# Performance work log

Hardware: AMD Instinct MI355X
Metric: run time of the kernel (lower is better)

Reference implementation:

```python
import jax, jax.numpy as jnp
import numpy as np

B, T, I = 8, 8192, 512
E, K, J = 16, 1024, 512

def setup_inputs() -> dict:
    key = jax.random.key(0)
    k1, k2, k3 = jax.random.split(key, 3)
    x = jax.random.normal(k1, (B, T, I), dtype=jnp.float32)
    Ind = jax.random.randint(k2, (B, E, K), 0, T, dtype=jnp.int32)
    bound = 1.0 / np.sqrt(I)
    W = jax.random.uniform(k3, (E, I, J), dtype=jnp.float32, minval=-bound, maxval=bound)
    return {"x": x, "Ind": Ind, "W": W}

def reference(x, Ind, W):
    # gather: [B,E,K,I] = x[b, Ind[b,e,k], :]
    gathered = jnp.take_along_axis(x[:, None, :, :], Ind[:, :, :, None], axis=2)
    # per-expert GEMM: [B,E,K,J]
    return jnp.einsum('beki,eij->bekj', gathered, W)
```

## Files before the change

### kernel.cpp

```cpp
#include <hip/hip_runtime.h>
#include <stdint.h>

typedef short short8 __attribute__((ext_vector_type(8)));
typedef float floatx16 __attribute__((ext_vector_type(16)));

constexpr int CB = 8;
constexpr int CT = 8192;
constexpr int CI = 512;
constexpr int CE = 16;
constexpr int CK = 1024;
constexpr int CJ = 512;

__device__ __forceinline__ uint32_t f2bf(float f) {
    union { float f; uint32_t u; } c; c.f = f;
    return (c.u + 0x7fffu + ((c.u >> 16) & 1u)) >> 16;
}
__device__ __forceinline__ uint32_t pack2(float lo, float hi) {
    return f2bf(lo) | (f2bf(hi) << 16);
}

__global__ __launch_bounds__(256, 2) void eg_kernel(
    const float* __restrict__ x, const int* __restrict__ Ind,
    const float* __restrict__ W, float* __restrict__ out)
{
    constexpr int AS_STRIDE = 20;
    constexpr int BS_STRIDE = 132;

    __shared__ __align__(16) uint32_t As[128 * AS_STRIDE];
    __shared__ __align__(16) uint32_t Bs[16 * BS_STRIDE];
    __shared__ int s_idx[128];

    const int t = threadIdx.x;
    const int z = blockIdx.z;
    const int e = z & (CE - 1);
    const int b = z >> 4;
    const int mtile = blockIdx.y;
    const int ntile = blockIdx.x;

    if (t < 128) s_idx[t] = Ind[z * CK + mtile * 128 + t];
    __syncthreads();

    const int am = t >> 1;
    const int ah = t & 1;
    const float* aptr = x + ((size_t)b * CT + s_idx[am]) * CI + ah * 16;
    uint32_t* adst = &As[am * AS_STRIDE + ah * 8];

    const int bjc = t & 31;
    const int bkp = t >> 5;
    const float* wptr = W + (size_t)e * CI * CJ + ntile * 128 + bjc * 4;

    const int ln = t & 63, wv = t >> 6;
    const int wm = (wv >> 1) * 64, wn = (wv & 1) * 64;
    const int lrow = ln & 31;
    const int lh = ln >> 5;

    const floatx16 fz = {0.f,0.f,0.f,0.f,0.f,0.f,0.f,0.f,0.f,0.f,0.f,0.f,0.f,0.f,0.f,0.f};
    floatx16 acc[2][2] = {{fz, fz}, {fz, fz}};

    for (int kt = 0; kt < CI / 32; ++kt) {
        {
            const float4* ap = (const float4*)(aptr + kt * 32);
            float4 a0 = ap[0], a1 = ap[1], a2 = ap[2], a3 = ap[3];
            uint4 w0 = make_uint4(pack2(a0.x, a0.y), pack2(a0.z, a0.w),
                                  pack2(a1.x, a1.y), pack2(a1.z, a1.w));
            uint4 w1 = make_uint4(pack2(a2.x, a2.y), pack2(a2.z, a2.w),
                                  pack2(a3.x, a3.y), pack2(a3.z, a3.w));
            ((uint4*)adst)[0] = w0;
            *((uint4*)(adst + 4)) = w1;
        }
        #pragma unroll
        for (int i = 0; i < 2; ++i) {
            const int kp = bkp + i * 8;
            const float* wp = wptr + (size_t)(kt * 32 + kp * 2) * CJ;
            float4 r0 = *(const float4*)(wp);
            float4 r1 = *(const float4*)(wp + CJ);
            uint4 wq = make_uint4(pack2(r0.x, r1.x), pack2(r0.y, r1.y),
                                  pack2(r0.z, r1.z), pack2(r0.w, r1.w));
            *((uint4*)&Bs[kp * BS_STRIDE + bjc * 4]) = wq;
        }
        __syncthreads();

        #pragma unroll
        for (int sub = 0; sub < 2; ++sub) {
            short8 af[2], bf[2];
            #pragma unroll
            for (int mt = 0; mt < 2; ++mt)
                af[mt] = *(const short8*)&As[(wm + mt * 32 + lrow) * AS_STRIDE + sub * 8 + lh * 4];
            #pragma unroll
            for (int nt = 0; nt < 2; ++nt) {
                const int n = wn + nt * 32 + lrow;
                const int kp0 = sub * 8 + lh * 4;
                union { uint32_t u[4]; short8 s; } cv;
                cv.u[0] = Bs[(kp0 + 0) * BS_STRIDE + n];
                cv.u[1] = Bs[(kp0 + 1) * BS_STRIDE + n];
                cv.u[2] = Bs[(kp0 + 2) * BS_STRIDE + n];
                cv.u[3] = Bs[(kp0 + 3) * BS_STRIDE + n];
                bf[nt] = cv.s;
            }
            #pragma unroll
            for (int mt = 0; mt < 2; ++mt)
                #pragma unroll
                for (int nt = 0; nt < 2; ++nt)
                    acc[mt][nt] = __builtin_amdgcn_mfma_f32_32x32x16_bf16(
                        af[mt], bf[nt], acc[mt][nt], 0, 0, 0);
        }
        __syncthreads();
    }

    const size_t obase = (size_t)z * CK * CJ;
    #pragma unroll
    for (int mt = 0; mt < 2; ++mt) {
        const int gm0 = mtile * 128 + wm + mt * 32 + lh * 4;
        #pragma unroll
        for (int nt = 0; nt < 2; ++nt) {
            const int gn = ntile * 128 + wn + nt * 32 + lrow;
            #pragma unroll
            for (int r = 0; r < 16; ++r) {
                const int gm = gm0 + (r & 3) + 8 * (r >> 2);
                out[obase + (size_t)gm * CJ + gn] = acc[mt][nt][r];
            }
        }
    }
}

extern "C" void kernel_launch(void* const* d_in, const int* in_sizes, int n_in,
                              void* d_out, int out_size, void* d_ws, size_t ws_size,
                              hipStream_t stream) {
    const float* x   = (const float*)d_in[0];
    const int*   Ind = (const int*)d_in[1];
    const float* W   = (const float*)d_in[2];
    float* out = (float*)d_out;

    dim3 grid(CJ / 128, CK / 128, CB * CE);
    dim3 block(256);
    hipLaunchKernelGGL(eg_kernel, grid, block, 0, stream, x, Ind, W, out);
}
```

Measured before the change: 510.8 us.

## Pre-convert inputs to bf16 and stream tiles via direct global-to-LDS loads

Adds two pre-pass kernels that convert x and W to bf16 in every call, with W repacked into a K-pair-interleaved tile layout. The GEMM kernel then loads 64-wide K tiles straight into LDS with global_load_lds, using an XOR swizzle on the A tile to avoid bank conflicts, and does fewer synchronisations per K step. This removes the per-tile fp32 loads and conversions in the main kernel and halves the bytes it reads. In exchange, a full pass converting x (128 MB) and W runs on every call, and the launch bound is raised to 4 blocks per CU.

```diff
diff --git a/kernel.cpp b/kernel.cpp
--- a/kernel.cpp
+++ b/kernel.cpp
@@ -11,6 +11,9 @@
 constexpr int CK = 1024;
 constexpr int CJ = 512;
 
+__device__ uint32_t g_xb[(size_t)CB * CT * CI / 2];
+__device__ uint32_t g_wb[(size_t)CE * CI * CJ / 2];
+
 __device__ __forceinline__ uint32_t f2bf(float f) {
     union { float f; uint32_t u; } c; c.f = f;
     return (c.u + 0x7fffu + ((c.u >> 16) & 1u)) >> 16;
@@ -19,15 +22,47 @@
     return f2bf(lo) | (f2bf(hi) << 16);
 }
 
-__global__ __launch_bounds__(256, 2) void eg_kernel(
-    const float* __restrict__ x, const int* __restrict__ Ind,
-    const float* __restrict__ W, float* __restrict__ out)
+__device__ __forceinline__ void gl_lds16(const uint32_t* g, uint32_t* l) {
+    __builtin_amdgcn_global_load_lds(
+        (const __attribute__((address_space(1))) uint32_t*)g,
+        (__attribute__((address_space(3))) uint32_t*)l,
+        16, 0, 0);
+}
+
+__global__ __launch_bounds__(256) void cvt_x(const float* __restrict__ x,
+                                             uint32_t* __restrict__ xb) {
+    size_t i = (size_t)blockIdx.x * 256 + threadIdx.x;
+    const float4* src = (const float4*)x;
+    float4 a = src[2 * i], b = src[2 * i + 1];
+    ((uint4*)xb)[i] = make_uint4(pack2(a.x, a.y), pack2(a.z, a.w),
+                                 pack2(b.x, b.y), pack2(b.z, b.w));
+}
+
+__global__ __launch_bounds__(256) void cvt_w(const float* __restrict__ W,
+                                             uint32_t* __restrict__ wb) {
+    uint32_t tid = blockIdx.x * 256 + threadIdx.x;
+    int jn  = tid & 127;
+    int kpq = (tid >> 7) & 7;
+    int kt  = (tid >> 10) & 7;
+    int nt  = (tid >> 13) & 3;
+    int e   = tid >> 15;
+    int n   = nt * 128 + jn;
+    int k0  = kt * 64 + kpq * 8;
+    const float* src = W + ((size_t)e * CI + k0) * CJ + n;
+    uint4 o;
+    o.x = pack2(src[0 * CJ], src[1 * CJ]);
+    o.y = pack2(src[2 * CJ], src[3 * CJ]);
+    o.z = pack2(src[4 * CJ], src[5 * CJ]);
+    o.w = pack2(src[6 * CJ], src[7 * CJ]);
+    ((uint4*)wb)[tid] = o;
+}
+
+__global__ __launch_bounds__(256, 4) void eg_kernel(
+    const uint32_t* __restrict__ xb, const int* __restrict__ Ind,
+    const uint32_t* __restrict__ wb, float* __restrict__ out)
 {
-    constexpr int AS_STRIDE = 20;
-    constexpr int BS_STRIDE = 132;
-
-    __shared__ __align__(16) uint32_t As[128 * AS_STRIDE];
-    __shared__ __align__(16) uint32_t Bs[16 * BS_STRIDE];
+    __shared__ __align__(16) uint32_t As[128 * 32];
+    __shared__ __align__(16) uint32_t Bs[32 * 128];
     __shared__ int s_idx[128];
 
     const int t = threadIdx.x;
@@ -40,16 +75,19 @@
     if (t < 128) s_idx[t] = Ind[z * CK + mtile * 128 + t];
     __syncthreads();
 
-    const int am = t >> 1;
-    const int ah = t & 1;
-    const float* aptr = x + ((size_t)b * CT + s_idx[am]) * CI + ah * 16;
-    uint32_t* adst = &As[am * AS_STRIDE + ah * 8];
+    const int ln = t & 63, wv = t >> 6;
 
-    const int bjc = t & 31;
-    const int bkp = t >> 5;
-    const float* wptr = W + (size_t)e * CI * CJ + ntile * 128 + bjc * 4;
+    const int sr = ln >> 3;
+    const int gchunk = (ln & 7) ^ sr;
+    const uint32_t* xb_b = xb + (size_t)b * CT * 256;
+    const uint32_t* pA[4];
+    #pragma unroll
+    for (int i = 0; i < 4; ++i) {
+        int r = wv * 32 + i * 8 + sr;
+        pA[i] = xb_b + (size_t)s_idx[r] * 256 + gchunk * 4;
+    }
+    const uint32_t* pB = wb + ((size_t)(e * 4 + ntile) * 8) * 4096 + wv * 1024 + ln * 4;
 
-    const int ln = t & 63, wv = t >> 6;
     const int wm = (wv >> 1) * 64, wn = (wv & 1) * 64;
     const int lrow = ln & 31;
     const int lh = ln >> 5;
@@ -57,52 +95,35 @@
     const floatx16 fz = {0.f,0.f,0.f,0.f,0.f,0.f,0.f,0.f,0.f,0.f,0.f,0.f,0.f,0.f,0.f,0.f};
     floatx16 acc[2][2] = {{fz, fz}, {fz, fz}};
 
-    for (int kt = 0; kt < CI / 32; ++kt) {
-        {
-            const float4* ap = (const float4*)(aptr + kt * 32);
-            float4 a0 = ap[0], a1 = ap[1], a2 = ap[2], a3 = ap[3];
-            uint4 w0 = make_uint4(pack2(a0.x, a0.y), pack2(a0.z, a0.w),
-                                  pack2(a1.x, a1.y), pack2(a1.z, a1.w));
-            uint4 w1 = make_uint4(pack2(a2.x, a2.y), pack2(a2.z, a2.w),
-                                  pack2(a3.x, a3.y), pack2(a3.z, a3.w));
-            ((uint4*)adst)[0] = w0;
-            *((uint4*)(adst + 4)) = w1;
-        }
+    for (int kt = 0; kt < 8; ++kt) {
         #pragma unroll
-        for (int i = 0; i < 2; ++i) {
-            const int kp = bkp + i * 8;
-            const float* wp = wptr + (size_t)(kt * 32 + kp * 2) * CJ;
-            float4 r0 = *(const float4*)(wp);
-            float4 r1 = *(const float4*)(wp + CJ);
-            uint4 wq = make_uint4(pack2(r0.x, r1.x), pack2(r0.y, r1.y),
-                                  pack2(r0.z, r1.z), pack2(r0.w, r1.w));
-            *((uint4*)&Bs[kp * BS_STRIDE + bjc * 4]) = wq;
-        }
+        for (int i = 0; i < 4; ++i)
+            gl_lds16(pA[i] + kt * 32, &As[wv * 1024 + i * 256]);
+        #pragma unroll
+        for (int i = 0; i < 4; ++i)
+            gl_lds16(pB + (size_t)kt * 4096 + i * 256, &Bs[wv * 1024 + i * 256]);
         __syncthreads();
 
         #pragma unroll
-        for (int sub = 0; sub < 2; ++sub) {
-            short8 af[2], bf[2];
+        for (int s = 0; s < 4; ++s) {
+            short8 af[2], bfr[2];
             #pragma unroll
-            for (int mt = 0; mt < 2; ++mt)
-                af[mt] = *(const short8*)&As[(wm + mt * 32 + lrow) * AS_STRIDE + sub * 8 + lh * 4];
+            for (int mt = 0; mt < 2; ++mt) {
+                const int row = wm + mt * 32 + lrow;
+                const int ch = (s * 2 + lh) ^ (lrow & 7);
+                af[mt] = *(const short8*)&As[row * 32 + ch * 4];
+            }
             #pragma unroll
             for (int nt = 0; nt < 2; ++nt) {
-                const int n = wn + nt * 32 + lrow;
-                const int kp0 = sub * 8 + lh * 4;
-                union { uint32_t u[4]; short8 s; } cv;
-                cv.u[0] = Bs[(kp0 + 0) * BS_STRIDE + n];
-                cv.u[1] = Bs[(kp0 + 1) * BS_STRIDE + n];
-                cv.u[2] = Bs[(kp0 + 2) * BS_STRIDE + n];
-                cv.u[3] = Bs[(kp0 + 3) * BS_STRIDE + n];
-                bf[nt] = cv.s;
+                const int jn = wn + nt * 32 + lrow;
+                bfr[nt] = *(const short8*)&Bs[(s * 2 + lh) * 512 + jn * 4];
             }
             #pragma unroll
             for (int mt = 0; mt < 2; ++mt)
                 #pragma unroll
                 for (int nt = 0; nt < 2; ++nt)
                     acc[mt][nt] = __builtin_amdgcn_mfma_f32_32x32x16_bf16(
-                        af[mt], bf[nt], acc[mt][nt], 0, 0, 0);
+                        af[mt], bfr[nt], acc[mt][nt], 0, 0, 0);
         }
         __syncthreads();
     }
@@ -131,7 +152,12 @@
     const float* W   = (const float*)d_in[2];
     float* out = (float*)d_out;
 
+    uint32_t* xb; hipGetSymbolAddress((void**)&xb, HIP_SYMBOL(g_xb));
+    uint32_t* wb; hipGetSymbolAddress((void**)&wb, HIP_SYMBOL(g_wb));
+
+    hipLaunchKernelGGL(cvt_x, dim3(CB * CT * CI / 8 / 256), dim3(256), 0, stream, x, xb);
+    hipLaunchKernelGGL(cvt_w, dim3(CE * CI * CJ / 8 / 256), dim3(256), 0, stream, W, wb);
+
     dim3 grid(CJ / 128, CK / 128, CB * CE);
-    dim3 block(256);
-    hipLaunchKernelGGL(eg_kernel, grid, block, 0, stream, x, Ind, W, out);
+    hipLaunchKernelGGL(eg_kernel, grid, dim3(256), 0, stream, xb, Ind, wb, out);
 }
```

Result: faster. 477.6 us (-6.5%).
